# Kernel tuning notes

Measured on AMD Instinct MI355X. Metric: run time of the kernel, lower is better.

The kernel has to match this reference:

```python
import jax, jax.numpy as jnp
import numpy as np
from jax import lax

R = 2  # upscale factor


def setup_inputs() -> dict:
    key = jax.random.key(0)
    k1, k2, k3 = jax.random.split(key, 3)
    x = jax.random.normal(k1, (16, 192, 192, 64), dtype=jnp.float32)
    # Conv2D kernel: HWIO, filters = r*r*64 = 256
    W = jax.random.normal(k2, (3, 3, 64, 256), dtype=jnp.float32) * 0.05
    b = jax.random.normal(k3, (256,), dtype=jnp.float32) * 0.05
    return {"x": x, "W": W, "b": b}


def reference(x, W, b):
    # Conv2D, stride 1, 'same' padding, NHWC/HWIO
    y = lax.conv_general_dilated(
        x, W, window_strides=(1, 1), padding="SAME",
        dimension_numbers=("NHWC", "HWIO", "NHWC")) + b
    # phase_shift: O[B, i*r+q, j*r+p, k] = y[B, i, j, k*r*r + p*r + q]
    B, a, bdim, c = y.shape
    cp = c // (R * R)
    y = y.reshape(B, a, bdim, cp, R, R)          # [B,a,b,k,p,q]
    y = jnp.transpose(y, (0, 1, 5, 2, 4, 3))     # [B,a,q,b,p,k]
    return y.reshape(B, a * R, bdim * R, cp)
```

## Files before the change

kernel.cpp:

```cpp
#include <hip/hip_runtime.h>
#include <stdint.h>

typedef short bf16x8 __attribute__((ext_vector_type(8)));
typedef float f32x4  __attribute__((ext_vector_type(4)));

#define GLOAD_LDS16(gp, lp) \
    __builtin_amdgcn_global_load_lds((const __attribute__((address_space(1))) void*)(gp), \
                                     (__attribute__((address_space(3))) void*)(lp), 16, 0, 0)

__device__ __forceinline__ uint32_t bfbits(float f) {
    uint32_t u = __builtin_bit_cast(uint32_t, f);
    u += 0x7FFFu + ((u >> 16) & 1u);
    return u >> 16;
}
__device__ __forceinline__ uint32_t pk2(float a, float b) {
    return bfbits(a) | (bfbits(b) << 16);
}

__global__ void prep_kernel(const float* __restrict__ x, short* __restrict__ xb,
                            const float* __restrict__ W, short* __restrict__ Wt) {
    const int b = blockIdx.x;
    if (b < 2048) {
        const int total = 16 * 194 * 194 * 8;
        for (int i = b * 256 + threadIdx.x; i < total; i += 2048 * 256) {
            int g  = i & 7;
            int t  = i >> 3;
            int wp = t % 194; t /= 194;
            int hp = t % 194;
            int nn = t / 194;
            uint4 r = {0u, 0u, 0u, 0u};
            if (hp >= 1 && hp <= 192 && wp >= 1 && wp <= 192) {
                const float* s = x + (((size_t)nn * 192 + (hp - 1)) * 192 + (wp - 1)) * 64 + g * 8;
                f32x4 a = __builtin_nontemporal_load((const f32x4*)s);
                f32x4 bb = __builtin_nontemporal_load((const f32x4*)(s + 4));
                r.x = pk2(a[0], a[1]); r.y = pk2(a[2], a[3]);
                r.z = pk2(bb[0], bb[1]); r.w = pk2(bb[2], bb[3]);
            }
            *(uint4*)(xb + (size_t)i * 8) = r;
        }
    } else {
        int idx = (b - 2048) * 256 + threadIdx.x;
        if (idx < 147456) {
            int t  = idx >> 14;
            int r  = idx & 16383;
            int c  = r >> 12;
            int j  = (r >> 6) & 63;
            int ic = r & 63;
            Wt[idx] = (short)bfbits(W[(t * 64 + ic) * 256 + j * 4 + c]);
        }
    }
}

#define NT 6
#define RING 10
#define A_SLOT 4224
#define A_SH   (RING * A_SLOT)
#define B_SH   (9 * 64 * 64)

__global__ __launch_bounds__(512, 2) void conv_ps_kernel(
    const short* __restrict__ xb, const short* __restrict__ Wt,
    const float* __restrict__ bias, float* __restrict__ out)
{
    __shared__ short smem[A_SH + B_SH];
    short* As = smem;
    short* Bs = smem + A_SH;

    const int tid   = threadIdx.x;
    const int lane  = tid & 63;
    const int wv    = tid >> 6;
    const int row_l = lane & 15;
    const int grp   = lane >> 4;
    const int b7    = row_l & 7;

    const int raw = blockIdx.x;
    const int lb  = (raw & 7) * 96 + (raw >> 3);
    const int c   = lb & 3;
    const int wt  = (lb >> 2) % 3;
    const int hg  = (lb / 12) & 3;
    const int n   = lb / 48;
    const int w0  = wt * 64;
    const int hbase = hg * 48;
    const int q = c & 1, p = (c >> 1) & 1;

    for (int k = wv; k < 90; k += 8) {
        int rl  = k / 9, jj = k % 9;
        int row = hbase - 1 + rl;
        int slot = (row + 1) % RING;
        int cch = jj * 64 + lane;
        int wpos = cch >> 3, g1 = cch & 7;
        int gs   = g1 ^ (wpos & 7);
        const short* src = xb + (((size_t)n * 194 + (row + 1)) * 194 + (w0 + wpos)) * 64 + gs * 8;
        void* dst = (char*)As + slot * 8448 + jj * 1024;
        if (jj < 8)            GLOAD_LDS16(src, dst);
        else if (lane < 16)    GLOAD_LDS16(src, dst);
    }
    {
        const short* wsrc = Wt + c * 4096;
        for (int k = wv; k < 72; k += 8) {
            int t   = k >> 3, j8 = k & 7;
            int cch = j8 * 64 + lane;
            int j   = cch >> 3, s1 = cch & 7;
            int ss  = s1 ^ (j & 7);
            GLOAD_LDS16(wsrc + t * 16384 + j * 64 + ss * 8,
                        (char*)Bs + t * 8192 + j8 * 1024);
        }
    }
    __syncthreads();

    f32x4 bv4[4];
    #pragma unroll
    for (int nt = 0; nt < 4; ++nt) {
        const int j0 = nt * 16 + grp * 4;
        #pragma unroll
        for (int jv = 0; jv < 4; ++jv)
            bv4[nt][jv] = bias[(j0 + jv) * 4 + c];
    }

    #pragma unroll 1
    for (int it = 0; it < NT; ++it) {
        const int h0 = hbase + it * 8;

        f32x4 acc[4][4];
        #pragma unroll
        for (int i = 0; i < 4; ++i)
            #pragma unroll
            for (int j = 0; j < 4; ++j)
                acc[i][j] = bv4[j];

        int sl[3];
        #pragma unroll
        for (int dy = 0; dy < 3; ++dy) sl[dy] = (h0 + wv + dy) % RING;

        #pragma unroll
        for (int dy = 0; dy < 3; ++dy) {
            #pragma unroll
            for (int dx = 0; dx < 3; ++dx) {
                const int t  = dy * 3 + dx;
                const int rd = row_l + dx;
                const int a7 = rd & 7;
                const int aB = sl[dy] * A_SLOT + rd * 64;
                const int bB = t * 4096 + row_l * 64;
                #pragma unroll
                for (int ks = 0; ks < 2; ++ks) {
                    const int kg = ks * 4 + grp;
                    const short* ap = &As[aB + ((kg ^ a7) << 3)];
                    const short* bp = &Bs[bB + ((kg ^ b7) << 3)];
                    bf16x8 af[4], bfr[4];
                    #pragma unroll
                    for (int mt = 0; mt < 4; ++mt) af[mt]  = *(const bf16x8*)(ap + mt * 1024);
                    #pragma unroll
                    for (int nt = 0; nt < 4; ++nt) bfr[nt] = *(const bf16x8*)(bp + nt * 1024);
                    #pragma unroll
                    for (int mt = 0; mt < 4; ++mt)
                        #pragma unroll
                        for (int nt = 0; nt < 4; ++nt)
                            acc[mt][nt] = __builtin_amdgcn_mfma_f32_16x16x32_bf16(
                                bfr[nt], af[mt], acc[mt][nt], 0, 0, 0);
                }
            }
        }

        const int h = h0 + wv;
        const long rowb = ((long)(n * 384 + 2 * h + q)) * 384;

        if (it < NT - 1) {
            asm volatile("s_waitcnt lgkmcnt(0)" ::: "memory");
            __builtin_amdgcn_sched_barrier(0);
            __builtin_amdgcn_s_barrier();
            __builtin_amdgcn_sched_barrier(0);

            for (int k = wv; k < 72; k += 8) {
                int rl  = k / 9, jj = k % 9;
                int row = h0 + 9 + rl;
                int slot = (row + 1) % RING;
                int cch = jj * 64 + lane;
                int wpos = cch >> 3, g1 = cch & 7;
                int gs   = g1 ^ (wpos & 7);
                const short* src = xb + (((size_t)n * 194 + (row + 1)) * 194 + (w0 + wpos)) * 64 + gs * 8;
                void* dst = (char*)As + slot * 8448 + jj * 1024;
                if (jj < 8)         GLOAD_LDS16(src, dst);
                else if (lane < 16) GLOAD_LDS16(src, dst);
            }
            asm volatile("" ::: "memory");
            __builtin_amdgcn_sched_barrier(0);

            #pragma unroll
            for (int mt = 0; mt < 4; ++mt) {
                float* po = out + ((rowb + 2 * (w0 + mt * 16 + row_l) + p) * 64 + grp * 4);
                #pragma unroll
                for (int nt = 0; nt < 4; ++nt)
                    __builtin_nontemporal_store(acc[mt][nt], (f32x4*)(po + nt * 16));
            }

            asm volatile("s_waitcnt vmcnt(15)" ::: "memory");
            __builtin_amdgcn_sched_barrier(0);
            __builtin_amdgcn_s_barrier();
            __builtin_amdgcn_sched_barrier(0);
        } else {
            #pragma unroll
            for (int mt = 0; mt < 4; ++mt) {
                float* po = out + ((rowb + 2 * (w0 + mt * 16 + row_l) + p) * 64 + grp * 4);
                #pragma unroll
                for (int nt = 0; nt < 4; ++nt)
                    __builtin_nontemporal_store(acc[mt][nt], (f32x4*)(po + nt * 16));
            }
        }
    }
}

extern "C" void kernel_launch(void* const* d_in, const int* in_sizes, int n_in,
                              void* d_out, int out_size, void* d_ws, size_t ws_size,
                              hipStream_t stream) {
    const float* x = (const float*)d_in[0];
    const float* W = (const float*)d_in[1];
    const float* b = (const float*)d_in[2];
    float* out = (float*)d_out;

    const size_t xb_bytes = (size_t)16 * 194 * 194 * 64 * 2;
    short* xbuf = (short*)d_ws;
    short* Wt   = (short*)((char*)d_ws + xb_bytes);

    hipLaunchKernelGGL(prep_kernel, dim3(2624), dim3(256), 0, stream, x, xbuf, W, Wt);
    hipLaunchKernelGGL(conv_ps_kernel, dim3(768), dim3(512), 0, stream, xbuf, Wt, b, out);
}
```

Measured before the change: 235.6 us.

## Stream weight taps through double buffer and shrink blocks to 4 waves

Instead of keeping all 9 weight taps resident in LDS, the kernel streams one tap at a time through a two-slot LDS buffer, prefetching the next tap while the current one computes. The activation ring shrinks to 7 rows, and blocks drop to 256 threads over 24-row segments with twice as many blocks. The goal is to cut LDS footprint so more blocks fit per CU and loads overlap with MFMA work. In exchange there are 9 barriers per iteration and weights are reloaded from global memory every tile.

```diff
diff --git a/kernel.cpp b/kernel.cpp
--- a/kernel.cpp
+++ b/kernel.cpp
@@ -51,19 +51,16 @@
     }
 }
 
-#define NT 6
-#define RING 10
-#define A_SLOT 4224
-#define A_SH   (RING * A_SLOT)
-#define B_SH   (9 * 64 * 64)
-
-__global__ __launch_bounds__(512, 2) void conv_ps_kernel(
+#define NRING 7
+#define ASLOT_B 8448
+#define B_OFF   (NRING * ASLOT_B)
+#define SMEM_SHORTS ((B_OFF + 2 * 8192) / 2)
+
+__global__ __launch_bounds__(256, 2) void conv_ps_kernel(
     const short* __restrict__ xb, const short* __restrict__ Wt,
     const float* __restrict__ bias, float* __restrict__ out)
 {
-    __shared__ short smem[A_SH + B_SH];
-    short* As = smem;
-    short* Bs = smem + A_SH;
+    __shared__ short smem[SMEM_SHORTS];
 
     const int tid   = threadIdx.x;
     const int lane  = tid & 63;
@@ -73,38 +70,50 @@
     const int b7    = row_l & 7;
 
     const int raw = blockIdx.x;
-    const int lb  = (raw & 7) * 96 + (raw >> 3);
-    const int c   = lb & 3;
-    const int wt  = (lb >> 2) % 3;
-    const int hg  = (lb / 12) & 3;
-    const int n   = lb / 48;
-    const int w0  = wt * 64;
-    const int hbase = hg * 48;
+    const int lb  = (raw & 7) * 192 + (raw >> 3);
+    const int c    = lb & 3;
+    const int wt   = (lb >> 2) % 3;
+    const int hseg = (lb / 12) % 8;
+    const int n    = lb / 96;
+    const int w0   = wt * 64;
+    const int hbase = hseg * 24;
     const int q = c & 1, p = (c >> 1) & 1;
 
-    for (int k = wv; k < 90; k += 8) {
-        int rl  = k / 9, jj = k % 9;
-        int row = hbase - 1 + rl;
-        int slot = (row + 1) % RING;
-        int cch = jj * 64 + lane;
-        int wpos = cch >> 3, g1 = cch & 7;
-        int gs   = g1 ^ (wpos & 7);
-        const short* src = xb + (((size_t)n * 194 + (row + 1)) * 194 + (w0 + wpos)) * 64 + gs * 8;
-        void* dst = (char*)As + slot * 8448 + jj * 1024;
-        if (jj < 8)            GLOAD_LDS16(src, dst);
-        else if (lane < 16)    GLOAD_LDS16(src, dst);
-    }
-    {
-        const short* wsrc = Wt + c * 4096;
-        for (int k = wv; k < 72; k += 8) {
-            int t   = k >> 3, j8 = k & 7;
-            int cch = j8 * 64 + lane;
-            int j   = cch >> 3, s1 = cch & 7;
-            int ss  = s1 ^ (j & 7);
-            GLOAD_LDS16(wsrc + t * 16384 + j * 64 + ss * 8,
-                        (char*)Bs + t * 8192 + j8 * 1024);
-        }
-    }
+    const short* wsrc = Wt + c * 4096;
+
+    auto issueB = [&](int tap, int buf) {
+        #pragma unroll
+        for (int r = 0; r < 2; ++r) {
+            int cch = tid + r * 256;
+            int j = cch >> 3, s = cch & 7, ss = s ^ (j & 7);
+            GLOAD_LDS16(wsrc + tap * 16384 + j * 64 + ss * 8,
+                        (char*)smem + B_OFF + buf * 8192 + (wv * 64 + r * 256) * 16);
+        }
+    };
+    auto issueA = [&](int row) {
+        int rowc = row > 192 ? 192 : row;
+        int slot = (row + 1) % NRING;
+        size_t rbase = ((size_t)n * 194 + (rowc + 1)) * 194;
+        #pragma unroll
+        for (int r = 0; r < 2; ++r) {
+            int cch = wv * 132 + r * 64 + lane;
+            int wpos = cch >> 3, g = cch & 7, gs = g ^ (wpos & 7);
+            GLOAD_LDS16(xb + (rbase + (w0 + wpos)) * 64 + gs * 8,
+                        (char*)smem + slot * ASLOT_B + (wv * 132 + r * 64) * 16);
+        }
+        if (lane < 4) {
+            int cch = wv * 132 + 128 + lane;
+            int wpos = cch >> 3, g = cch & 7, gs = g ^ (wpos & 7);
+            GLOAD_LDS16(xb + (rbase + (w0 + wpos)) * 64 + gs * 8,
+                        (char*)smem + slot * ASLOT_B + (wv * 132 + 128) * 16);
+        }
+    };
+
+    issueB(0, 0);
+    #pragma unroll
+    for (int r = 0; r < 5; ++r) issueA(hbase - 1 + r);
+    asm volatile("s_waitcnt vmcnt(0)" ::: "memory");
+    __builtin_amdgcn_sched_barrier(0);
     __syncthreads();
 
     f32x4 bv4[4];
@@ -116,9 +125,42 @@
             bv4[nt][jv] = bias[(j0 + jv) * 4 + c];
     }
 
+#define TAP_HDR() \
+    __builtin_amdgcn_s_barrier(); \
+    __builtin_amdgcn_sched_barrier(0);
+#define TAP_SYNC(VMN) \
+    __builtin_amdgcn_sched_barrier(0); \
+    asm volatile("s_waitcnt vmcnt(" #VMN ")" ::: "memory"); \
+    __builtin_amdgcn_sched_barrier(0); \
+    __builtin_amdgcn_s_barrier(); \
+    __builtin_amdgcn_sched_barrier(0);
+
+#define COMPUTE_TAP(DY, DX, BUF) { \
+    const int rd = row_l + (DX); \
+    const int a7 = rd & 7; \
+    const int aB = sl[DY] * 4224 + rd * 64; \
+    const short* bbase = smem + B_OFF / 2 + (BUF) * 4096 + row_l * 64; \
+    _Pragma("unroll") for (int ks = 0; ks < 2; ++ks) { \
+        const int kg = ks * 4 + grp; \
+        const short* ap = &smem[aB + ((kg ^ a7) << 3)]; \
+        const short* bp = bbase + ((kg ^ b7) << 3); \
+        bf16x8 af[4], bfr[4]; \
+        _Pragma("unroll") for (int mt = 0; mt < 4; ++mt) af[mt]  = *(const bf16x8*)(ap + mt * 1024); \
+        _Pragma("unroll") for (int nt = 0; nt < 4; ++nt) bfr[nt] = *(const bf16x8*)(bp + nt * 1024); \
+        _Pragma("unroll") for (int mt = 0; mt < 4; ++mt) \
+            _Pragma("unroll") for (int nt = 0; nt < 4; ++nt) \
+                acc[mt][nt] = __builtin_amdgcn_mfma_f32_16x16x32_bf16( \
+                    bfr[nt], af[mt], acc[mt][nt], 0, 0, 0); \
+    } }
+
+    int pb = 0;
     #pragma unroll 1
-    for (int it = 0; it < NT; ++it) {
-        const int h0 = hbase + it * 8;
+    for (int it = 0; it < 6; ++it) {
+        const int h0 = hbase + it * 4;
+
+        int sl[3];
+        #pragma unroll
+        for (int dy = 0; dy < 3; ++dy) sl[dy] = (h0 + wv + dy) % NRING;
 
         f32x4 acc[4][4];
         #pragma unroll
@@ -127,63 +169,48 @@
             for (int j = 0; j < 4; ++j)
                 acc[i][j] = bv4[j];
 
-        int sl[3];
-        #pragma unroll
-        for (int dy = 0; dy < 3; ++dy) sl[dy] = (h0 + wv + dy) % RING;
-
-        #pragma unroll
-        for (int dy = 0; dy < 3; ++dy) {
-            #pragma unroll
-            for (int dx = 0; dx < 3; ++dx) {
-                const int t  = dy * 3 + dx;
-                const int rd = row_l + dx;
-                const int a7 = rd & 7;
-                const int aB = sl[dy] * A_SLOT + rd * 64;
-                const int bB = t * 4096 + row_l * 64;
-                #pragma unroll
-                for (int ks = 0; ks < 2; ++ks) {
-                    const int kg = ks * 4 + grp;
-                    const short* ap = &As[aB + ((kg ^ a7) << 3)];
-                    const short* bp = &Bs[bB + ((kg ^ b7) << 3)];
-                    bf16x8 af[4], bfr[4];
-                    #pragma unroll
-                    for (int mt = 0; mt < 4; ++mt) af[mt]  = *(const bf16x8*)(ap + mt * 1024);
-                    #pragma unroll
-                    for (int nt = 0; nt < 4; ++nt) bfr[nt] = *(const bf16x8*)(bp + nt * 1024);
-                    #pragma unroll
-                    for (int mt = 0; mt < 4; ++mt)
-                        #pragma unroll
-                        for (int nt = 0; nt < 4; ++nt)
-                            acc[mt][nt] = __builtin_amdgcn_mfma_f32_16x16x32_bf16(
-                                bfr[nt], af[mt], acc[mt][nt], 0, 0, 0);
-                }
-            }
-        }
-
-        const int h = h0 + wv;
-        const long rowb = ((long)(n * 384 + 2 * h + q)) * 384;
-
-        if (it < NT - 1) {
-            asm volatile("s_waitcnt lgkmcnt(0)" ::: "memory");
-            __builtin_amdgcn_sched_barrier(0);
-            __builtin_amdgcn_s_barrier();
-            __builtin_amdgcn_sched_barrier(0);
-
-            for (int k = wv; k < 72; k += 8) {
-                int rl  = k / 9, jj = k % 9;
-                int row = h0 + 9 + rl;
-                int slot = (row + 1) % RING;
-                int cch = jj * 64 + lane;
-                int wpos = cch >> 3, g1 = cch & 7;
-                int gs   = g1 ^ (wpos & 7);
-                const short* src = xb + (((size_t)n * 194 + (row + 1)) * 194 + (w0 + wpos)) * 64 + gs * 8;
-                void* dst = (char*)As + slot * 8448 + jj * 1024;
-                if (jj < 8)         GLOAD_LDS16(src, dst);
-                else if (lane < 16) GLOAD_LDS16(src, dst);
-            }
-            asm volatile("" ::: "memory");
-            __builtin_amdgcn_sched_barrier(0);
-
+        const int pA = pb, pBb = pb ^ 1;
+
+        TAP_HDR();
+        issueB(1, pBb); issueA(h0 + 4); issueA(h0 + 5);
+        TAP_SYNC(24);
+        COMPUTE_TAP(0, 0, pA);
+        TAP_HDR();
+        issueB(2, pA);
+        TAP_SYNC(8);
+        COMPUTE_TAP(0, 1, pBb);
+        TAP_HDR();
+        issueB(3, pBb);
+        TAP_SYNC(2);
+        COMPUTE_TAP(0, 2, pA);
+        TAP_HDR();
+        issueB(4, pA); issueA(h0 + 6);
+        TAP_SYNC(5);
+        COMPUTE_TAP(1, 0, pBb);
+        TAP_HDR();
+        issueB(5, pBb);
+        TAP_SYNC(5);
+        COMPUTE_TAP(1, 1, pA);
+        TAP_HDR();
+        issueB(6, pA);
+        TAP_SYNC(2);
+        COMPUTE_TAP(1, 2, pBb);
+        TAP_HDR();
+        issueB(7, pBb); issueA(h0 + 7);
+        TAP_SYNC(5);
+        COMPUTE_TAP(2, 0, pA);
+        TAP_HDR();
+        issueB(8, pA);
+        TAP_SYNC(5);
+        COMPUTE_TAP(2, 1, pBb);
+        TAP_HDR();
+        issueB(0, pBb);
+        TAP_SYNC(2);
+        COMPUTE_TAP(2, 2, pA);
+
+        {
+            const int h = h0 + wv;
+            const long rowb = ((long)(n * 384 + 2 * h + q)) * 384;
             #pragma unroll
             for (int mt = 0; mt < 4; ++mt) {
                 float* po = out + ((rowb + 2 * (w0 + mt * 16 + row_l) + p) * 64 + grp * 4);
@@ -191,21 +218,13 @@
                 for (int nt = 0; nt < 4; ++nt)
                     __builtin_nontemporal_store(acc[mt][nt], (f32x4*)(po + nt * 16));
             }
-
-            asm volatile("s_waitcnt vmcnt(15)" ::: "memory");
-            __builtin_amdgcn_sched_barrier(0);
-            __builtin_amdgcn_s_barrier();
-            __builtin_amdgcn_sched_barrier(0);
-        } else {
-            #pragma unroll
-            for (int mt = 0; mt < 4; ++mt) {
-                float* po = out + ((rowb + 2 * (w0 + mt * 16 + row_l) + p) * 64 + grp * 4);
-                #pragma unroll
-                for (int nt = 0; nt < 4; ++nt)
-                    __builtin_nontemporal_store(acc[mt][nt], (f32x4*)(po + nt * 16));
-            }
-        }
+        }
+
+        pb ^= 1;
     }
+#undef COMPUTE_TAP
+#undef TAP_HDR
+#undef TAP_SYNC
 }
 
 extern "C" void kernel_launch(void* const* d_in, const int* in_sizes, int n_in,
@@ -221,5 +240,5 @@
     short* Wt   = (short*)((char*)d_ws + xb_bytes);
 
     hipLaunchKernelGGL(prep_kernel, dim3(2624), dim3(256), 0, stream, x, xbuf, W, Wt);
-    hipLaunchKernelGGL(conv_ps_kernel, dim3(768), dim3(512), 0, stream, xbuf, Wt, b, out);
-}
+    hipLaunchKernelGGL(conv_ps_kernel, dim3(1536), dim3(256), 0, stream, xbuf, Wt, b, out);
+}
```

Measured after the change: 236.6 us. Within noise of the previous version (+0.4%).
